# Optimization experiments

Hardware: AMD Instinct MI355X
Metric: run time of the kernel (lower is better)

The kernel has to match this reference:

```python
import jax, jax.numpy as jnp
import numpy as np

B, H, W, DIM = 8, 32, 32, 768
HEADS = 12
HD = DIM // HEADS  # 64


def setup_inputs() -> dict:
    key = jax.random.key(0)
    ks = jax.random.split(key, 7)
    s = 0.02  # init scale to keep logits in a sane range
    return {
        "x": jax.random.normal(ks[0], (B, H, W, DIM), jnp.float32),
        "qkv_w": jax.random.normal(ks[1], (3 * DIM, DIM), jnp.float32) * s,
        "qkv_b": jax.random.normal(ks[2], (3 * DIM,), jnp.float32) * s,
        "proj_w": jax.random.normal(ks[3], (DIM, DIM), jnp.float32) * s,
        "proj_b": jax.random.normal(ks[4], (DIM,), jnp.float32) * s,
        "rel_pos_h": jax.random.normal(ks[5], (2 * H - 1, HD), jnp.float32) * s,
        "rel_pos_w": jax.random.normal(ks[6], (2 * W - 1, HD), jnp.float32) * s,
    }


def reference(x, qkv_w, qkv_b, proj_w, proj_b, rel_pos_h, rel_pos_w):
    b, h, w, dim = x.shape
    n = h * w
    hd = dim // HEADS
    scale = hd ** -0.5

    xf = x.reshape(b, n, dim)
    qkv = xf @ qkv_w.T + qkv_b                       # (B, N, 3*dim)
    qkv = qkv.reshape(b, n, 3, HEADS, hd)
    qkv = jnp.transpose(qkv, (2, 0, 3, 1, 4)).reshape(3, b * HEADS, n, hd)
    q, k, v = qkv[0], qkv[1], qkv[2]                 # each (B*heads, N, hd)

    # decomposed rel-pos bias (q_size == k_size -> pure index lookup)
    coords_h = jnp.arange(h)[:, None] - jnp.arange(h)[None, :] + (h - 1)
    coords_w = jnp.arange(w)[:, None] - jnp.arange(w)[None, :] + (w - 1)
    Rh = rel_pos_h[coords_h]                         # (H, H, hd)
    Rw = rel_pos_w[coords_w]                         # (W, W, hd)
    r_q = q.reshape(b * HEADS, h, w, hd)
    rel_h = jnp.einsum('bhwc,hkc->bhwk', r_q, Rh)    # (B*heads, H, W, H)
    rel_w = jnp.einsum('bhwc,wkc->bhwk', r_q, Rw)    # (B*heads, H, W, W)
    bias = (rel_h[:, :, :, :, None] + rel_w[:, :, :, None, :]).reshape(b * HEADS, n, n)

    attn = (q * scale) @ jnp.swapaxes(k, -2, -1) + bias
    attn = jax.nn.softmax(attn, axis=-1)
    out = attn @ v                                   # (B*heads, N, hd)

    out = out.reshape(b, HEADS, n, hd)
    out = jnp.transpose(out, (0, 2, 1, 3)).reshape(b, n, dim)
    out = out @ proj_w.T + proj_b
    return out.reshape(b, h, w, dim)
```

## Files before the change

kernel.cpp:

```cpp
#include <hip/hip_runtime.h>
#include <hip/hip_bf16.h>

typedef unsigned short u16;
typedef __attribute__((ext_vector_type(8))) short bf16x8;
typedef __attribute__((ext_vector_type(4))) short s16x4;
typedef __attribute__((ext_vector_type(4))) float f32x4;

#define QSCALE 0.18033688011116012f
#define RPSCALE 8.0f
#define EXP2(x) __builtin_amdgcn_exp2f(x)

__device__ __forceinline__ float bf2f(u16 u) {
  union { unsigned int i; float f; } v; v.i = ((unsigned int)u) << 16; return v.f;
}
__device__ __forceinline__ u16 f2bf(float f) {
  union { float f; unsigned int i; } v; v.f = f;
  unsigned int r = v.i + 0x7fffu + ((v.i >> 16) & 1u);
  return (u16)(r >> 16);
}
__device__ __forceinline__ unsigned int pk2bf(float a, float b) {
  union { __hip_bfloat162 h; unsigned int u; } cv;
  cv.h = __float22bfloat162_rn(float2{a, b});
  return cv.u;
}
__device__ __forceinline__ f32x4 MFMA(bf16x8 a, bf16x8 b, f32x4 c) {
  return __builtin_amdgcn_mfma_f32_16x16x32_bf16(a, b, c, 0, 0, 0);
}
__device__ __forceinline__ void cvt8(const float* p, uint4* dst) {
  float4 f0 = *(const float4*)(p);
  float4 f1 = *(const float4*)(p + 4);
  u16* t = (u16*)dst;
  t[0] = f2bf(f0.x); t[1] = f2bf(f0.y); t[2] = f2bf(f0.z); t[3] = f2bf(f0.w);
  t[4] = f2bf(f1.x); t[5] = f2bf(f1.y); t[6] = f2bf(f1.z); t[7] = f2bf(f1.w);
}
__device__ __forceinline__ void cvt8s(const float* p, uint4* dst, float s) {
  float4 f0 = *(const float4*)(p);
  float4 f1 = *(const float4*)(p + 4);
  u16* t = (u16*)dst;
  t[0] = f2bf(f0.x * s); t[1] = f2bf(f0.y * s); t[2] = f2bf(f0.z * s); t[3] = f2bf(f0.w * s);
  t[4] = f2bf(f1.x * s); t[5] = f2bf(f1.y * s); t[6] = f2bf(f1.z * s); t[7] = f2bf(f1.w * s);
}
__device__ __forceinline__ void gld16(const u16* g, u16* l) {
  __builtin_amdgcn_global_load_lds(
      (const __attribute__((address_space(1))) unsigned int*)g,
      (__attribute__((address_space(3))) unsigned int*)l, 16, 0, 0);
}

#define N8_X  786432
#define N8_QW 221184
#define N8_PW 73728
__global__ __launch_bounds__(256) void cast_kernel(
    const float* __restrict__ x, const float* __restrict__ qw, const float* __restrict__ pw,
    u16* __restrict__ xb, u16* __restrict__ qwb, u16* __restrict__ pwb)
{
  const int i = blockIdx.x * 256 + threadIdx.x;
  const float* s; u16* d; int off;
  if (i < N8_X)            { s = x;  d = xb;  off = i; }
  else if (i < N8_X+N8_QW) { s = qw; d = qwb; off = i - N8_X; }
  else                     { s = pw; d = pwb; off = i - (N8_X + N8_QW); }
  uint4 pk; cvt8(s + (size_t)off * 8, &pk);
  *(uint4*)(d + (size_t)off * 8) = pk;
}

template<int MODE, int NXB>
__global__ __launch_bounds__(256) void gemm_bt(
    const u16* __restrict__ A, const u16* __restrict__ Bw, const float* __restrict__ bias,
    void* __restrict__ C0v, u16* __restrict__ C1, u16* __restrict__ C2,
    int M, int N, int K)
{
  __shared__ u16 sA[128 * 32];
  __shared__ u16 sB[128 * 32];
  const int tid = threadIdx.x;
  const int lane = tid & 63, wv = tid >> 6;
  const int wr = wv >> 1, wc = wv & 1;
  const int l16 = lane & 15, quad = lane >> 4;
  const int bi = blockIdx.x;
  const int t = bi >> 3;
  const int nx = t % NXB;
  const int my = ((t / NXB) << 3) | (bi & 7);
  const int m0 = my << 7, n0 = nx << 7;

  const int srow = tid >> 2, scol = (tid & 3) << 3;
  const u16* gA0 = A  + (size_t)(m0 + srow) * K + scol;
  const u16* gB0 = Bw + (size_t)(n0 + srow) * K + scol;
  const u16* gA1 = gA0 + (size_t)64 * K;
  const u16* gB1 = gB0 + (size_t)64 * K;
  u16* const lwA0 = sA + wv * 512;
  u16* const lwA1 = sA + 2048 + wv * 512;
  u16* const lwB0 = sB + wv * 512;
  u16* const lwB1 = sB + 2048 + wv * 512;

  f32x4 acc[4][4];
  #pragma unroll
  for (int i = 0; i < 4; ++i)
    #pragma unroll
    for (int j = 0; j < 4; ++j) {
      acc[i][j][0] = 0.f; acc[i][j][1] = 0.f; acc[i][j][2] = 0.f; acc[i][j][3] = 0.f;
    }

  for (int k0 = 0; k0 < K; k0 += 32) {
    __syncthreads();
    gld16(gA0 + k0, lwA0);
    gld16(gA1 + k0, lwA1);
    gld16(gB0 + k0, lwB0);
    gld16(gB1 + k0, lwB1);
    __syncthreads();
    bf16x8 af[4], bfr[4];
    #pragma unroll
    for (int i = 0; i < 4; ++i)
      af[i] = *(const bf16x8*)(sA + (wr * 64 + i * 16 + l16) * 32 + quad * 8);
    #pragma unroll
    for (int j = 0; j < 4; ++j)
      bfr[j] = *(const bf16x8*)(sB + (wc * 64 + j * 16 + l16) * 32 + quad * 8);
    #pragma unroll
    for (int i = 0; i < 4; ++i)
      #pragma unroll
      for (int j = 0; j < 4; ++j)
        acc[i][j] = MFMA(af[i], bfr[j], acc[i][j]);
  }

  #pragma unroll
  for (int j = 0; j < 4; ++j) {
    const int n = n0 + wc * 64 + j * 16 + l16;
    const float bv = bias[n];
    if (MODE == 0) {
      float* C0 = (float*)C0v;
      #pragma unroll
      for (int i = 0; i < 4; ++i) {
        const int m = m0 + wr * 64 + i * 16 + quad * 4;
        #pragma unroll
        for (int r = 0; r < 4; ++r)
          C0[(size_t)(m + r) * N + n] = acc[i][j][r] + bv;
      }
    } else {
      u16* C0 = (u16*)C0v;
      const int which = n / 768;
      const int rem = n - which * 768;
      const int head = rem >> 6, c = rem & 63;
      #pragma unroll
      for (int i = 0; i < 4; ++i) {
        const int m = m0 + wr * 64 + i * 16 + quad * 4;
        const int b = m >> 10, npos = m & 1023;
        const size_t bh = (size_t)(b * 12 + head);
        if (which == 0) {
          #pragma unroll
          for (int r = 0; r < 4; ++r)
            C0[(bh << 16) + ((size_t)(npos + r) << 6) + c] =
                f2bf((acc[i][j][r] + bv) * QSCALE);
        } else if (which == 1) {
          const size_t base = ((bh * 16 + (size_t)(npos >> 6)) << 12)
                            + (size_t)((((npos >> 4) & 3) * 2 + (c >> 5)) << 9)
                            + (size_t)((((npos & 15) + 16 * ((c >> 3) & 3)) << 3) + (c & 7));
          #pragma unroll
          for (int r = 0; r < 4; ++r)
            C1[base + r * 8] = f2bf(acc[i][j][r] + bv);
        } else {
          const size_t base = ((bh * 16 + (size_t)(npos >> 6)) << 12)
                            + (size_t)(((((npos >> 5) & 1) * 4 + (c >> 4))) << 9)
                            + (size_t)((((c & 15) + 16 * ((npos >> 3) & 3)) << 3) + (npos & 7));
          s16x4 pk;
          #pragma unroll
          for (int r = 0; r < 4; ++r) pk[r] = (short)f2bf(acc[i][j][r] + bv);
          *(s16x4*)(C2 + base) = pk;
        }
      }
    }
  }
}

__global__ __launch_bounds__(256, 4) void attn_kernel(
    const u16* __restrict__ Q, const u16* __restrict__ Kf, const u16* __restrict__ Vf,
    const float* __restrict__ rph, const float* __restrict__ rpw,
    u16* __restrict__ Oa)
{
  __shared__ __align__(16) u16 uni[9216];
  __shared__ u16 sSh[4 * 16 * 36];

  u16* const uRPH = uni;
  u16* const uRPW = uni + 4536;

  const int tid = threadIdx.x;
  const int wave = tid >> 6, lane = tid & 63;
  const int l16 = lane & 15, quad = lane >> 4;
  const int bi = blockIdx.x;
  const int t = bi >> 3;
  const int qb = t & 15;
  const int bh = ((t >> 4) << 3) | (bi & 7);
  const int qrow0 = (qb << 6) + (wave << 4);
  const int qh = qrow0 >> 5;
  const int qwb = qrow0 & 31;

  u16* const pw = uni + wave * 1152;
  u16* const sShw = sSh + wave * 576;

  bf16x8 qf[2];
  {
    const u16* qp = Q + (((size_t)bh << 10) + qrow0 + l16) * 64 + quad * 8;
    qf[0] = *(const bf16x8*)(qp);
    qf[1] = *(const bf16x8*)(qp + 32);
  }

  for (int j = tid; j < 64 * 8; j += 256) {
    const int row = j >> 3, ck = (j & 7) << 3;
    uint4 vw;
    if (row < 63) cvt8s(rpw + (size_t)row * 64 + ck, &vw, RPSCALE);
    else { vw.x = 0u; vw.y = 0u; vw.z = 0u; vw.w = 0u; }
    *(uint4*)(uRPW + row * 72 + ck) = vw;
    if (row < 63) {
      uint4 vh;
      cvt8s(rph + (size_t)row * 64 + ck, &vh, RPSCALE);
      *(uint4*)(uRPH + row * 72 + ck) = vh;
    }
  }
  __syncthreads();

  #pragma unroll
  for (int tk = 0; tk < 2; ++tk) {
    const int kh = tk * 16 + l16;
    const u16* bp = uRPH + (qh + 31 - kh) * 72 + quad * 8;
    bf16x8 b0 = *(const bf16x8*)(bp);
    bf16x8 b1 = *(const bf16x8*)(bp + 32);
    f32x4 c; c[0] = 0.f; c[1] = 0.f; c[2] = 0.f; c[3] = 0.f;
    c = MFMA(qf[0], b0, c);
    c = MFMA(qf[1], b1, c);
    #pragma unroll
    for (int r = 0; r < 4; ++r)
      sShw[(quad * 4 + r) * 36 + tk * 16 + l16] = f2bf(c[r]);
  }

  f32x4 swc[4];
  #pragma unroll
  for (int tj = 0; tj < 4; ++tj) {
    const u16* bp = uRPW + (tj * 16 + l16) * 72 + quad * 8;
    bf16x8 b0 = *(const bf16x8*)(bp);
    bf16x8 b1 = *(const bf16x8*)(bp + 32);
    f32x4 c; c[0] = 0.f; c[1] = 0.f; c[2] = 0.f; c[3] = 0.f;
    c = MFMA(qf[0], b0, c);
    c = MFMA(qf[1], b1, c);
    swc[tj] = c;
  }
  __syncthreads();

  #pragma unroll
  for (int tj = 0; tj < 4; ++tj)
    #pragma unroll
    for (int r = 0; r < 4; ++r)
      pw[(quad * 4 + r) * 72 + tj * 16 + l16] = f2bf(swc[tj][r]);

  float rw[2][4];
  #pragma unroll
  for (int hi = 0; hi < 2; ++hi)
    #pragma unroll
    for (int r = 0; r < 4; ++r) {
      const int kw = hi * 16 + quad * 4 + r;
      rw[hi][r] = bf2f(pw[l16 * 72 + (qwb + l16 - kw + 31)]);
    }

  f32x4 oacc[4];
  #pragma unroll
  for (int nd = 0; nd < 4; ++nd) {
    oacc[nd][0] = 0.f; oacc[nd][1] = 0.f; oacc[nd][2] = 0.f; oacc[nd][3] = 0.f;
  }
  float lsum = 0.f;

  const u16* const Kfb = Kf + (((size_t)bh) << 16) + lane * 8;
  const u16* const Vfb = Vf + (((size_t)bh) << 16) + lane * 8;

  for (int kt = 0; kt < 16; ++kt) {
    const u16* Kp = Kfb + ((size_t)kt << 12);
    const u16* Vp = Vfb + ((size_t)kt << 12);
    bf16x8 kfr[8], vfr[8];
    #pragma unroll
    for (int m = 0; m < 8; ++m)
      kfr[m] = *(const bf16x8*)(Kp + (m << 9));
    #pragma unroll
    for (int m = 0; m < 8; ++m)
      vfr[m] = *(const bf16x8*)(Vp + (m << 9));
    float rh[2];
    {
      const unsigned int w2 =
          *(const unsigned int*)(sShw + l16 * 36 + (kt << 1));
      rh[0] = bf2f((u16)(w2 & 0xffffu));
      rh[1] = bf2f((u16)(w2 >> 16));
    }
    f32x4 sacc[4];
    #pragma unroll
    for (int mk = 0; mk < 4; ++mk) {
      f32x4 t4; t4[0] = 0.f; t4[1] = 0.f; t4[2] = 0.f; t4[3] = 0.f;
      t4 = MFMA(kfr[mk * 2 + 0], qf[0], t4);
      t4 = MFMA(kfr[mk * 2 + 1], qf[1], t4);
      sacc[mk] = t4;
    }
    #pragma unroll
    for (int mk = 0; mk < 4; ++mk) {
      const float rhv = rh[mk >> 1];
      const float* rwp = rw[mk & 1];
      float e0 = EXP2(sacc[mk][0] + rhv + rwp[0]);
      float e1 = EXP2(sacc[mk][1] + rhv + rwp[1]);
      float e2 = EXP2(sacc[mk][2] + rhv + rwp[2]);
      float e3 = EXP2(sacc[mk][3] + rhv + rwp[3]);
      lsum += (e0 + e1) + (e2 + e3);
      uint2 pk2; pk2.x = pk2bf(e0, e1); pk2.y = pk2bf(e2, e3);
      *(uint2*)(pw + l16 * 72 + mk * 16 + quad * 4) = pk2;
    }
    #pragma unroll
    for (int ks = 0; ks < 2; ++ks) {
      bf16x8 ap = *(const bf16x8*)(pw + l16 * 72 + ks * 32 + quad * 8);
      #pragma unroll
      for (int nd = 0; nd < 4; ++nd)
        oacc[nd] = MFMA(vfr[ks * 4 + nd], ap, oacc[nd]);
    }
  }

  lsum += __shfl_xor(lsum, 16);
  lsum += __shfl_xor(lsum, 32);

  const int b = bh / 12, head = bh - b * 12;
  const float linv = 1.0f / lsum;
  const size_t base =
      ((size_t)(b << 10) + qrow0 + l16) * 768 + head * 64 + quad * 4;
  #pragma unroll
  for (int nd = 0; nd < 4; ++nd) {
    s16x4 pk;
    #pragma unroll
    for (int r = 0; r < 4; ++r) pk[r] = (short)f2bf(oacc[nd][r] * linv);
    *(s16x4*)(Oa + base + nd * 16) = pk;
  }
}

extern "C" void kernel_launch(void* const* d_in, const int* in_sizes, int n_in,
                              void* d_out, int out_size, void* d_ws, size_t ws_size,
                              hipStream_t stream) {
  (void)in_sizes; (void)n_in; (void)out_size; (void)ws_size;
  const float* x      = (const float*)d_in[0];
  const float* qkv_w  = (const float*)d_in[1];
  const float* qkv_b  = (const float*)d_in[2];
  const float* proj_w = (const float*)d_in[3];
  const float* proj_b = (const float*)d_in[4];
  const float* rph    = (const float*)d_in[5];
  const float* rpw    = (const float*)d_in[6];
  float* out = (float*)d_out;

  char* ws = (char*)d_ws;
  const size_t SZ = (size_t)96 * 1024 * 64;
  u16* Qw  = (u16*)ws;
  u16* Kfw = Qw + SZ;
  u16* Vfw = Kfw + SZ;
  u16* Xb  = Vfw + SZ;
  u16* Oa  = Xb;
  u16* QWb = Xb + SZ;
  u16* PWb = QWb + (size_t)2304 * 768;

  cast_kernel<<<4224, 256, 0, stream>>>(x, qkv_w, proj_w, Xb, QWb, PWb);
  gemm_bt<1, 18><<<1152, 256, 0, stream>>>(Xb, QWb, qkv_b, Qw, Kfw, Vfw, 8192, 2304, 768);
  attn_kernel<<<1536, 256, 0, stream>>>(Qw, Kfw, Vfw, rph, rpw, Oa);
  gemm_bt<0, 6><<<384, 256, 0, stream>>>(Oa, PWb, proj_b, out, nullptr, nullptr, 8192, 768, 768);
}
```

Before: 232.8 us.

## Process two 16-row query tiles per wave to reuse K/V fragments

Each wave in the attention kernel now handles 32 query rows (two 16-row tiles) instead of 16, so each K and V fragment loaded from global memory feeds twice as many MFMAs. The grid shrinks from 1536 to 768 blocks, and the per-wave P and rel-pos scratch in LDS doubles. V loads move next to their use inside the PV stage to limit register pressure, and the launch bound no longer requests 4 blocks per SM. The aim is to halve K/V global traffic per query row, at the cost of more registers and LDS, lower occupancy, and fewer blocks to spread across CUs.

```diff
diff --git a/kernel.cpp b/kernel.cpp
--- a/kernel.cpp
+++ b/kernel.cpp
@@ -168,13 +168,13 @@
   }
 }
 
-__global__ __launch_bounds__(256, 4) void attn_kernel(
+__global__ __launch_bounds__(256) void attn_kernel(
     const u16* __restrict__ Q, const u16* __restrict__ Kf, const u16* __restrict__ Vf,
     const float* __restrict__ rph, const float* __restrict__ rpw,
     u16* __restrict__ Oa)
 {
   __shared__ __align__(16) u16 uni[9216];
-  __shared__ u16 sSh[4 * 16 * 36];
+  __shared__ u16 sSh[4 * 32 * 36];
 
   u16* const uRPH = uni;
   u16* const uRPW = uni + 4536;
@@ -184,20 +184,20 @@
   const int l16 = lane & 15, quad = lane >> 4;
   const int bi = blockIdx.x;
   const int t = bi >> 3;
-  const int qb = t & 15;
-  const int bh = ((t >> 4) << 3) | (bi & 7);
-  const int qrow0 = (qb << 6) + (wave << 4);
+  const int qb = t & 7;
+  const int bh = ((t >> 3) << 3) | (bi & 7);
+  const int qrow0 = (qb << 7) + (wave << 5);
   const int qh = qrow0 >> 5;
-  const int qwb = qrow0 & 31;
-
-  u16* const pw = uni + wave * 1152;
-  u16* const sShw = sSh + wave * 576;
-
-  bf16x8 qf[2];
-  {
-    const u16* qp = Q + (((size_t)bh << 10) + qrow0 + l16) * 64 + quad * 8;
-    qf[0] = *(const bf16x8*)(qp);
-    qf[1] = *(const bf16x8*)(qp + 32);
+
+  u16* const pw = uni + wave * 2304;
+  u16* const sShw = sSh + wave * 1152;
+
+  bf16x8 qf[2][2];
+  #pragma unroll
+  for (int qt = 0; qt < 2; ++qt) {
+    const u16* qp = Q + (((size_t)bh << 10) + qrow0 + qt * 16 + l16) * 64 + quad * 8;
+    qf[qt][0] = *(const bf16x8*)(qp);
+    qf[qt][1] = *(const bf16x8*)(qp + 32);
   }
 
   for (int j = tid; j < 64 * 8; j += 256) {
@@ -215,53 +215,64 @@
   __syncthreads();
 
   #pragma unroll
-  for (int tk = 0; tk < 2; ++tk) {
-    const int kh = tk * 16 + l16;
-    const u16* bp = uRPH + (qh + 31 - kh) * 72 + quad * 8;
-    bf16x8 b0 = *(const bf16x8*)(bp);
-    bf16x8 b1 = *(const bf16x8*)(bp + 32);
-    f32x4 c; c[0] = 0.f; c[1] = 0.f; c[2] = 0.f; c[3] = 0.f;
-    c = MFMA(qf[0], b0, c);
-    c = MFMA(qf[1], b1, c);
-    #pragma unroll
-    for (int r = 0; r < 4; ++r)
-      sShw[(quad * 4 + r) * 36 + tk * 16 + l16] = f2bf(c[r]);
-  }
-
-  f32x4 swc[4];
-  #pragma unroll
-  for (int tj = 0; tj < 4; ++tj) {
-    const u16* bp = uRPW + (tj * 16 + l16) * 72 + quad * 8;
-    bf16x8 b0 = *(const bf16x8*)(bp);
-    bf16x8 b1 = *(const bf16x8*)(bp + 32);
-    f32x4 c; c[0] = 0.f; c[1] = 0.f; c[2] = 0.f; c[3] = 0.f;
-    c = MFMA(qf[0], b0, c);
-    c = MFMA(qf[1], b1, c);
-    swc[tj] = c;
-  }
+  for (int qt = 0; qt < 2; ++qt)
+    #pragma unroll
+    for (int tk = 0; tk < 2; ++tk) {
+      const int kh = tk * 16 + l16;
+      const u16* bp = uRPH + (qh + 31 - kh) * 72 + quad * 8;
+      bf16x8 b0 = *(const bf16x8*)(bp);
+      bf16x8 b1 = *(const bf16x8*)(bp + 32);
+      f32x4 c; c[0] = 0.f; c[1] = 0.f; c[2] = 0.f; c[3] = 0.f;
+      c = MFMA(qf[qt][0], b0, c);
+      c = MFMA(qf[qt][1], b1, c);
+      #pragma unroll
+      for (int r = 0; r < 4; ++r)
+        sShw[(qt * 16 + quad * 4 + r) * 36 + tk * 16 + l16] = f2bf(c[r]);
+    }
+
+  f32x4 swc[2][4];
+  #pragma unroll
+  for (int qt = 0; qt < 2; ++qt)
+    #pragma unroll
+    for (int tj = 0; tj < 4; ++tj) {
+      const u16* bp = uRPW + (tj * 16 + l16) * 72 + quad * 8;
+      bf16x8 b0 = *(const bf16x8*)(bp);
+      bf16x8 b1 = *(const bf16x8*)(bp + 32);
+      f32x4 c; c[0] = 0.f; c[1] = 0.f; c[2] = 0.f; c[3] = 0.f;
+      c = MFMA(qf[qt][0], b0, c);
+      c = MFMA(qf[qt][1], b1, c);
+      swc[qt][tj] = c;
+    }
   __syncthreads();
 
   #pragma unroll
-  for (int tj = 0; tj < 4; ++tj)
-    #pragma unroll
-    for (int r = 0; r < 4; ++r)
-      pw[(quad * 4 + r) * 72 + tj * 16 + l16] = f2bf(swc[tj][r]);
-
-  float rw[2][4];
-  #pragma unroll
-  for (int hi = 0; hi < 2; ++hi)
-    #pragma unroll
-    for (int r = 0; r < 4; ++r) {
-      const int kw = hi * 16 + quad * 4 + r;
-      rw[hi][r] = bf2f(pw[l16 * 72 + (qwb + l16 - kw + 31)]);
-    }
-
-  f32x4 oacc[4];
-  #pragma unroll
-  for (int nd = 0; nd < 4; ++nd) {
-    oacc[nd][0] = 0.f; oacc[nd][1] = 0.f; oacc[nd][2] = 0.f; oacc[nd][3] = 0.f;
-  }
-  float lsum = 0.f;
+  for (int qt = 0; qt < 2; ++qt)
+    #pragma unroll
+    for (int tj = 0; tj < 4; ++tj)
+      #pragma unroll
+      for (int r = 0; r < 4; ++r)
+        pw[(qt * 16 + quad * 4 + r) * 72 + tj * 16 + l16] = f2bf(swc[qt][tj][r]);
+
+  float rw[2][2][4];
+  #pragma unroll
+  for (int qt = 0; qt < 2; ++qt)
+    #pragma unroll
+    for (int hi = 0; hi < 2; ++hi)
+      #pragma unroll
+      for (int r = 0; r < 4; ++r) {
+        const int kw = hi * 16 + quad * 4 + r;
+        rw[qt][hi][r] = bf2f(pw[(qt * 16 + l16) * 72 + (qt * 16 + l16 - kw + 31)]);
+      }
+
+  f32x4 oacc[2][4];
+  #pragma unroll
+  for (int qt = 0; qt < 2; ++qt)
+    #pragma unroll
+    for (int nd = 0; nd < 4; ++nd) {
+      oacc[qt][nd][0] = 0.f; oacc[qt][nd][1] = 0.f;
+      oacc[qt][nd][2] = 0.f; oacc[qt][nd][3] = 0.f;
+    }
+  float lsum[2] = {0.f, 0.f};
 
   const u16* const Kfb = Kf + (((size_t)bh) << 16) + lane * 8;
   const u16* const Vfb = Vf + (((size_t)bh) << 16) + lane * 8;
@@ -269,62 +280,79 @@
   for (int kt = 0; kt < 16; ++kt) {
     const u16* Kp = Kfb + ((size_t)kt << 12);
     const u16* Vp = Vfb + ((size_t)kt << 12);
-    bf16x8 kfr[8], vfr[8];
+    bf16x8 kfr[8];
     #pragma unroll
     for (int m = 0; m < 8; ++m)
       kfr[m] = *(const bf16x8*)(Kp + (m << 9));
     #pragma unroll
     for (int m = 0; m < 8; ++m)
-      vfr[m] = *(const bf16x8*)(Vp + (m << 9));
-    float rh[2];
-    {
+      asm volatile("" :: "v"(kfr[m]));
+
+    float rh[2][2];
+    #pragma unroll
+    for (int qt = 0; qt < 2; ++qt) {
       const unsigned int w2 =
-          *(const unsigned int*)(sShw + l16 * 36 + (kt << 1));
-      rh[0] = bf2f((u16)(w2 & 0xffffu));
-      rh[1] = bf2f((u16)(w2 >> 16));
-    }
-    f32x4 sacc[4];
-    #pragma unroll
-    for (int mk = 0; mk < 4; ++mk) {
-      f32x4 t4; t4[0] = 0.f; t4[1] = 0.f; t4[2] = 0.f; t4[3] = 0.f;
-      t4 = MFMA(kfr[mk * 2 + 0], qf[0], t4);
-      t4 = MFMA(kfr[mk * 2 + 1], qf[1], t4);
-      sacc[mk] = t4;
-    }
-    #pragma unroll
-    for (int mk = 0; mk < 4; ++mk) {
-      const float rhv = rh[mk >> 1];
-      const float* rwp = rw[mk & 1];
-      float e0 = EXP2(sacc[mk][0] + rhv + rwp[0]);
-      float e1 = EXP2(sacc[mk][1] + rhv + rwp[1]);
-      float e2 = EXP2(sacc[mk][2] + rhv + rwp[2]);
-      float e3 = EXP2(sacc[mk][3] + rhv + rwp[3]);
-      lsum += (e0 + e1) + (e2 + e3);
-      uint2 pk2; pk2.x = pk2bf(e0, e1); pk2.y = pk2bf(e2, e3);
-      *(uint2*)(pw + l16 * 72 + mk * 16 + quad * 4) = pk2;
-    }
+          *(const unsigned int*)(sShw + (qt * 16 + l16) * 36 + (kt << 1));
+      rh[qt][0] = bf2f((u16)(w2 & 0xffffu));
+      rh[qt][1] = bf2f((u16)(w2 >> 16));
+    }
+
+    #pragma unroll
+    for (int qt = 0; qt < 2; ++qt) {
+      f32x4 sacc[4];
+      #pragma unroll
+      for (int mk = 0; mk < 4; ++mk) {
+        f32x4 t4; t4[0] = 0.f; t4[1] = 0.f; t4[2] = 0.f; t4[3] = 0.f;
+        t4 = MFMA(kfr[mk * 2 + 0], qf[qt][0], t4);
+        t4 = MFMA(kfr[mk * 2 + 1], qf[qt][1], t4);
+        sacc[mk] = t4;
+      }
+      #pragma unroll
+      for (int mk = 0; mk < 4; ++mk) {
+        const float rhv = rh[qt][mk >> 1];
+        const float* rwp = rw[qt][mk & 1];
+        float e0 = EXP2(sacc[mk][0] + rhv + rwp[0]);
+        float e1 = EXP2(sacc[mk][1] + rhv + rwp[1]);
+        float e2 = EXP2(sacc[mk][2] + rhv + rwp[2]);
+        float e3 = EXP2(sacc[mk][3] + rhv + rwp[3]);
+        lsum[qt] += (e0 + e1) + (e2 + e3);
+        uint2 pk2; pk2.x = pk2bf(e0, e1); pk2.y = pk2bf(e2, e3);
+        *(uint2*)(pw + (qt * 16 + l16) * 72 + mk * 16 + quad * 4) = pk2;
+      }
+    }
+
     #pragma unroll
     for (int ks = 0; ks < 2; ++ks) {
-      bf16x8 ap = *(const bf16x8*)(pw + l16 * 72 + ks * 32 + quad * 8);
+      bf16x8 bv[4];
       #pragma unroll
       for (int nd = 0; nd < 4; ++nd)
-        oacc[nd] = MFMA(vfr[ks * 4 + nd], ap, oacc[nd]);
-    }
-  }
-
-  lsum += __shfl_xor(lsum, 16);
-  lsum += __shfl_xor(lsum, 32);
+        bv[nd] = *(const bf16x8*)(Vp + ((ks * 4 + nd) << 9));
+      #pragma unroll
+      for (int qt = 0; qt < 2; ++qt) {
+        bf16x8 ap = *(const bf16x8*)(pw + (qt * 16 + l16) * 72 + ks * 32 + quad * 8);
+        #pragma unroll
+        for (int nd = 0; nd < 4; ++nd)
+          oacc[qt][nd] = MFMA(bv[nd], ap, oacc[qt][nd]);
+      }
+    }
+  }
 
   const int b = bh / 12, head = bh - b * 12;
-  const float linv = 1.0f / lsum;
-  const size_t base =
-      ((size_t)(b << 10) + qrow0 + l16) * 768 + head * 64 + quad * 4;
-  #pragma unroll
-  for (int nd = 0; nd < 4; ++nd) {
-    s16x4 pk;
-    #pragma unroll
-    for (int r = 0; r < 4; ++r) pk[r] = (short)f2bf(oacc[nd][r] * linv);
-    *(s16x4*)(Oa + base + nd * 16) = pk;
+  #pragma unroll
+  for (int qt = 0; qt < 2; ++qt) {
+    float ls = lsum[qt];
+    ls += __shfl_xor(ls, 16);
+    ls += __shfl_xor(ls, 32);
+    const float linv = 1.0f / ls;
+    const size_t base =
+        ((size_t)(b << 10) + qrow0 + qt * 16 + l16) * 768 + head * 64 + quad * 4;
+    #pragma unroll
+    for (int nd = 0; nd < 4; ++nd) {
+      s16x4 pk;
+      #pragma unroll
+      for (int r = 0; r < 4; ++r) pk[r] = (short)f2bf(oacc[qt][nd][r] * linv);
+      *(s16x4*)(Oa + base + nd * 16) = pk;
+    }
   }
 }
 
@@ -353,6 +381,6 @@
 
   cast_kernel<<<4224, 256, 0, stream>>>(x, qkv_w, proj_w, Xb, QWb, PWb);
   gemm_bt<1, 18><<<1152, 256, 0, stream>>>(Xb, QWb, qkv_b, Qw, Kfw, Vfw, 8192, 2304, 768);
-  attn_kernel<<<1536, 256, 0, stream>>>(Qw, Kfw, Vfw, rph, rpw, Oa);
+  attn_kernel<<<768, 256, 0, stream>>>(Qw, Kfw, Vfw, rph, rpw, Oa);
   gemm_bt<0, 6><<<384, 256, 0, stream>>>(Oa, PWb, proj_b, out, nullptr, nullptr, 8192, 768, 768);
 }
```

After: 211.8 us. 9.0% less time.
